# Kernel optimization log

Measured on AMD Instinct MI355X. Metric: run time of the kernel, lower is better.

Reference implementation:

```python
import jax, jax.numpy as jnp
import numpy as np

THRESH = 0.7  # similarity_threshold from __init__
EPS = 1e-8    # torch cosine_similarity eps


def setup_inputs() -> dict:
    key = jax.random.key(0)
    ks = jax.random.split(key, 7)
    B, D, F, H, M, NMEM = 65536, 512, 10, 512, 256, 1024
    return {
        "query_features": jax.random.normal(ks[0], (B, D), jnp.float32),
        "B_mat": jax.random.normal(ks[1], (D, F), jnp.float32),
        "W1": jax.random.normal(ks[2], (2 * F, H), jnp.float32) * 0.05,
        "b1": jax.random.normal(ks[3], (H,), jnp.float32) * 0.01,
        "W2": jax.random.normal(ks[4], (H, M), jnp.float32) * 0.05,
        "b2": jax.random.normal(ks[5], (M,), jnp.float32) * 0.01,
        "memory_bank": jax.random.normal(ks[6], (NMEM, M), jnp.float32),
    }


def reference(query_features, B_mat, W1, b1, W2, b2, memory_bank):
    # Fourier features (eq. 8): [B, 2F]
    xp = query_features @ B_mat
    ff = jnp.concatenate([jnp.sin(xp), jnp.cos(xp)], axis=-1)
    # memory_net MLP -> query vectors [B, M]
    h = jax.nn.relu(ff @ W1 + b1)
    q = h @ W2 + b2
    # cosine similarity q vs memory bank (torch semantics: dot / max(|a||b|, eps))
    qn = jnp.linalg.norm(q, axis=-1, keepdims=True)          # [B,1]
    mn = jnp.linalg.norm(memory_bank, axis=-1, keepdims=True)  # [N,1]
    sim = (q @ memory_bank.T) / jnp.maximum(qn * mn.T, EPS)   # [B,N]
    max_sim = jnp.max(sim, axis=1)                            # [B]
    max_idx = jnp.argmax(sim, axis=1)                         # [B]
    relevant = memory_bank[max_idx]                           # [B,M] gather
    relevant = jnp.where((max_sim < THRESH)[:, None], 0.0, relevant)
    return relevant
```

## Files before the change

### kernel.cpp

```cpp
#include <hip/hip_runtime.h>
#include <hip/hip_bf16.h>


typedef __attribute__((ext_vector_type(8))) short short8;
typedef __attribute__((ext_vector_type(4))) float f32x4;

#define MFMA(a, b, c) __builtin_amdgcn_mfma_f32_16x16x32_bf16((a), (b), (c), 0, 0, 0)

static __device__ __forceinline__ short bfb(float f) {
  return (short)__builtin_bit_cast(unsigned short, __float2bfloat16(f));
}
static __device__ __forceinline__ unsigned short bf16bits(float f) {
  return __builtin_bit_cast(unsigned short, __float2bfloat16(f));
}
static __device__ __forceinline__ float sel10(const float a[10], int i) {
  float v = a[0];
#pragma unroll
  for (int j = 1; j < 10; ++j) v = (i == j) ? a[j] : v;
  return v;
}

typedef const __attribute__((address_space(1))) unsigned int* gas_p;
typedef __attribute__((address_space(3))) unsigned int* las_p;
static __device__ __forceinline__ void async16(const void* g, void* l) {
  __builtin_amdgcn_global_load_lds((gas_p)g, (las_p)l, 16, 0, 0);
}

__global__ __launch_bounds__(256) void prep_ff_kernel(
    const float* __restrict__ W1, const float* __restrict__ b1,
    const float* __restrict__ W2, const float* __restrict__ mem,
    const float* __restrict__ query, const float* __restrict__ Bmat,
    __hip_bfloat16* __restrict__ W1p, __hip_bfloat16* __restrict__ W2p,
    __hip_bfloat16* __restrict__ Mp, __hip_bfloat16* __restrict__ ff) {
  __shared__ __align__(16) float Bl[10 * 512];
  const int b = blockIdx.x, tid = threadIdx.x;
  if (b < 16) {
    float* invl = Bl;
    const int w = tid >> 6, lane = tid & 63, g = lane >> 4, jj = lane & 15;
    {
      int r = w * 16 + jj;
      const float4* m4 = (const float4*)(mem + (size_t)(b * 64 + r) * 256);
      float ss = 0.f;
      for (int t = 0; t < 16; ++t) {
        float4 v = m4[g * 16 + t];
        ss += v.x * v.x + v.y * v.y + v.z * v.z + v.w * v.w;
      }
      ss += __shfl_xor(ss, 16);
      ss += __shfl_xor(ss, 32);
      if (g == 0) invl[r] = rsqrtf(fmaxf(ss, 1e-30f));
    }
    __syncthreads();
    for (int u = 0; u < 64; ++u) {
      int t = u * 256 + tid;
      int j = t & 7, lane2 = (t >> 3) & 63, kt = (t >> 9) & 7, nl = t >> 12;
      int g2 = lane2 >> 4, jp = lane2 & 15;
      int nloc = nl * 16 + jp;
      int kap = 32 * kt + 16 * (j >> 2) + 4 * g2 + (j & 3);
      float v = mem[(size_t)(b * 64 + nloc) * 256 + kap] * invl[nloc];
      Mp[(size_t)b * 16384 + t] = __float2bfloat16(v);
    }
  } else if (b == 16) {
    for (int idx = tid; idx < 16384; idx += 256) {
      int j = idx & 7, lane2 = (idx >> 3) & 63, ct = idx >> 9;
      int g2 = lane2 >> 4, jp = lane2 & 15;
      int k = 8 * g2 + j;
      float v = 0.f;
      if (k < 20) v = W1[k * 512 + ct * 16 + jp];
      else if (k == 20) v = b1[ct * 16 + jp];
      W1p[idx] = __float2bfloat16(v);
    }
  } else if (b < 33) {
    int bb = b - 17;
    for (int u = 0; u < 32; ++u) {
      int idx = bb * 8192 + u * 256 + tid;
      int j = idx & 7, lane2 = (idx >> 3) & 63, c = (idx >> 9) & 15, kt = idx >> 13;
      int g2 = lane2 >> 4, jp = lane2 & 15;
      int kap = 32 * kt + 16 * (j >> 2) + 4 * g2 + (j & 3);
      W2p[idx] = __float2bfloat16(W2[(size_t)kap * 256 + c * 16 + jp]);
    }
  } else {
    const int bb = b - 33;
    for (int i = tid; i < 5120; i += 256) {
      int d = i / 10, f = i - d * 10;
      Bl[f * 512 + d] = Bmat[i];
    }
    __syncthreads();
    const int wv = tid >> 6, lane = tid & 63;
    const int g = lane >> 4, jj = lane & 15;
    const long r0 = (long)bb * 32 + (wv * 4 + g) * 2;
    const float4* qa = (const float4*)(query + r0 * 512);
    const float4* qb = (const float4*)(query + (r0 + 1) * 512);

    float acc[2][10];
#pragma unroll
    for (int f = 0; f < 10; ++f) { acc[0][f] = 0.f; acc[1][f] = 0.f; }
#pragma unroll
    for (int k = 0; k < 8; ++k) {
      float4 va = qa[jj + 16 * k];
      float4 vb = qb[jj + 16 * k];
#pragma unroll
      for (int f = 0; f < 10; ++f) {
        float4 bv = *(const float4*)(Bl + f * 512 + 4 * (jj + 16 * k));
        acc[0][f] = fmaf(va.x, bv.x, fmaf(va.y, bv.y, fmaf(va.z, bv.z, fmaf(va.w, bv.w, acc[0][f]))));
        acc[1][f] = fmaf(vb.x, bv.x, fmaf(vb.y, bv.y, fmaf(vb.z, bv.z, fmaf(vb.w, bv.w, acc[1][f]))));
      }
    }
#pragma unroll
    for (int r = 0; r < 2; ++r) {
#pragma unroll
      for (int f = 0; f < 10; ++f) {
        float s = acc[r][f];
        s += __shfl_xor(s, 1); s += __shfl_xor(s, 2);
        s += __shfl_xor(s, 4); s += __shfl_xor(s, 8);
        acc[r][f] = s;
      }
      int base = (jj < 5) ? 2 * jj : 2 * jj - 10;
      float a0 = sel10(acc[r], base);
      float a1 = sel10(acc[r], base + 1);
      float v0 = 0.f, v1 = 0.f;
      if (jj < 5) { v0 = sinf(a0); v1 = sinf(a1); }
      else if (jj < 10) { v0 = cosf(a0); v1 = cosf(a1); }
      else if (jj == 10) { v0 = 1.0f; }
      ushort2 pk;
      pk.x = bf16bits(v0);
      pk.y = bf16bits(v1);
      ((ushort2*)ff)[(r0 + r) * 16 + jj] = pk;
    }
  }
}

#define WAITV(N) asm volatile("s_waitcnt vmcnt(" #N ")" ::: "memory")
#define BAR()                        \
  do {                               \
    __builtin_amdgcn_s_barrier();    \
    asm volatile("" ::: "memory");   \
  } while (0)

#define STAGE_SLAB(s, bi)                                                       \
  do {                                                                          \
    const char* sp_ = ((s) < 32) ? (const char*)W2p + (size_t)(s) * 8192        \
                                 : (const char*)Mp + ((size_t)(s) - 32) * 8192; \
    char* dp_ = lds + 33792 + (bi) * 8192;                                      \
    async16(sp_ + tid * 16, dp_ + tid * 16);                                    \
    async16(sp_ + 4096 + tid * 16, dp_ + 4096 + tid * 16);                      \
  } while (0)

#define G3_EVEN(t, bi)                                                          \
  do {                                                                          \
    const char* buf = lds + 33792 + (bi) * 8192;                                \
    short8 a0 = *(const short8*)(lds + (size_t)(t) * 1024 + lane * 16);         \
    short8 a1 = *(const short8*)(lds + (size_t)((t) + 1) * 1024 + lane * 16);   \
    f32x4 d00 = MFMA(a0, ffq0, z4);                                             \
    f32x4 d01 = MFMA(a1, ffq0, z4);                                             \
    f32x4 d10 = MFMA(a0, ffq1, z4);                                             \
    f32x4 d11 = MFMA(a1, ffq1, z4);                                             \
    _Pragma("unroll") for (int i = 0; i < 4; ++i) {                             \
      hf0[i] = bfb(d00[i] > 0.f ? d00[i] : 0.f);                                \
      hf0[4 + i] = bfb(d01[i] > 0.f ? d01[i] : 0.f);                            \
      hf1[i] = bfb(d10[i] > 0.f ? d10[i] : 0.f);                                \
      hf1[4 + i] = bfb(d11[i] > 0.f ? d11[i] : 0.f);                            \
    }                                                                           \
    _Pragma("unroll") for (int c = 0; c < 8; ++c) {                             \
      short8 bfr = *(const short8*)(buf + c * 1024 + lane * 16);                \
      acc3a[c] = MFMA(bfr, hf0, acc3a[c]);                                      \
      acc3b[c] = MFMA(bfr, hf1, acc3b[c]);                                      \
    }                                                                           \
  } while (0)

#define G3_ODD(bi)                                                              \
  do {                                                                          \
    const char* buf = lds + 33792 + (bi) * 8192;                                \
    _Pragma("unroll") for (int c = 0; c < 8; ++c) {                             \
      short8 bfr = *(const short8*)(buf + c * 1024 + lane * 16);                \
      acc3a[8 + c] = MFMA(bfr, hf0, acc3a[8 + c]);                              \
      acc3b[8 + c] = MFMA(bfr, hf1, acc3b[8 + c]);                              \
    }                                                                           \
  } while (0)

#define G4(t, bi)                                                               \
  do {                                                                          \
    const char* buf = lds + 33792 + (bi) * 8192;                                \
    f32x4 a40 = z4, a41 = z4;                                                   \
    _Pragma("unroll") for (int kt = 0; kt < 8; ++kt) {                          \
      short8 bfr = *(const short8*)(buf + kt * 1024 + lane * 16);               \
      a40 = MFMA(qfrag0[kt], bfr, a40);                                         \
      a41 = MFMA(qfrag1[kt], bfr, a41);                                         \
    }                                                                           \
    const int n_ = ((t) - 32) * 16 + jj;                                        \
    _Pragma("unroll") for (int i = 0; i < 4; ++i) {                             \
      if (a40[i] > runmax0[i]) { runmax0[i] = a40[i]; runidx0[i] = n_; }        \
      if (a41[i] > runmax1[i]) { runmax1[i] = a41[i]; runidx1[i] = n_; }        \
    }                                                                           \
  } while (0)

__global__ __launch_bounds__(256, 2) void mega_kernel(
    const __hip_bfloat16* __restrict__ ff, const __hip_bfloat16* __restrict__ W1p,
    const __hip_bfloat16* __restrict__ W2p, const float* __restrict__ b2,
    const __hip_bfloat16* __restrict__ Mp, const float* __restrict__ mem,
    float* __restrict__ out) {
  __shared__ __align__(16) char lds[66560];
  const int tid = threadIdx.x, w = tid >> 6, lane = tid & 63;
  const int g = lane >> 4, jj = lane & 15;
  const int rowBase = blockIdx.x * 128 + w * 32;
  const f32x4 z4 = {0.f, 0.f, 0.f, 0.f};

  short8 ffq0 = *(const short8*)(ff + (size_t)(rowBase + jj) * 32 + g * 8);
  short8 ffq1 = *(const short8*)(ff + (size_t)(rowBase + 16 + jj) * 32 + g * 8);
  {
    float v = b2[tid];
    *(float*)(lds + 32768 + tid * 4) = v;
  }
#pragma unroll
  for (int r = 0; r < 8; ++r)
    async16((const char*)W1p + r * 4096 + tid * 16, lds + r * 4096 + tid * 16);
  STAGE_SLAB(0, 0);
  STAGE_SLAB(1, 1);
  STAGE_SLAB(2, 2);

  f32x4 acc3a[16], acc3b[16];
#pragma unroll
  for (int c = 0; c < 16; ++c) { acc3a[c] = z4; acc3b[c] = z4; }
  short8 hf0, hf1;

  for (int it = 0; it < 8; ++it) {
    const int t0 = it * 4;
    WAITV(4); BAR(); STAGE_SLAB(t0 + 3, 3); G3_EVEN(t0, 0);
    WAITV(4); BAR(); STAGE_SLAB(t0 + 4, 0); G3_ODD(1);
    WAITV(4); BAR(); STAGE_SLAB(t0 + 5, 1); G3_EVEN(t0 + 2, 2);
    WAITV(4); BAR(); STAGE_SLAB(t0 + 6, 2); G3_ODD(3);
  }

  short8 qfrag0[8], qfrag1[8];
  float invqn0, invqn1;
  {
    const float* b2l = (const float*)(lds + 32768);
    float qn0 = 0.f, qn1 = 0.f;
#pragma unroll
    for (int c = 0; c < 16; ++c) {
      f32x4 bb = *(const f32x4*)(b2l + c * 16 + 4 * g);
#pragma unroll
      for (int i = 0; i < 4; ++i) {
        float v0 = acc3a[c][i] + bb[i];
        float v1 = acc3b[c][i] + bb[i];
        qn0 += v0 * v0;
        qn1 += v1 * v1;
        qfrag0[c >> 1][(c & 1) * 4 + i] = bfb(v0);
        qfrag1[c >> 1][(c & 1) * 4 + i] = bfb(v1);
      }
    }
    qn0 += __shfl_xor(qn0, 16); qn0 += __shfl_xor(qn0, 32);
    qn1 += __shfl_xor(qn1, 16); qn1 += __shfl_xor(qn1, 32);
    invqn0 = rsqrtf(fmaxf(qn0, 1e-30f));
    invqn1 = rsqrtf(fmaxf(qn1, 1e-30f));
  }

  float runmax0[4], runmax1[4];
  int runidx0[4], runidx1[4];
#pragma unroll
  for (int i = 0; i < 4; ++i) {
    runmax0[i] = -1e30f; runidx0[i] = 0;
    runmax1[i] = -1e30f; runidx1[i] = 0;
  }

  for (int it = 0; it < 15; ++it) {
    const int t0 = 32 + it * 4;
    WAITV(4); BAR(); STAGE_SLAB(t0 + 3, 3); G4(t0, 0);
    WAITV(4); BAR(); STAGE_SLAB(t0 + 4, 0); G4(t0 + 1, 1);
    WAITV(4); BAR(); STAGE_SLAB(t0 + 5, 1); G4(t0 + 2, 2);
    WAITV(4); BAR(); STAGE_SLAB(t0 + 6, 2); G4(t0 + 3, 3);
  }
  WAITV(4); BAR(); STAGE_SLAB(95, 3); G4(92, 0);
  WAITV(4); BAR(); G4(93, 1);
  WAITV(2); BAR(); G4(94, 2);
  WAITV(0); BAR(); G4(95, 3);

  const float4* mem4 = (const float4*)mem;
  float4* out4 = (float4*)out;
#pragma unroll
  for (int rt = 0; rt < 2; ++rt) {
    float* rmax = rt ? runmax1 : runmax0;
    int* ridx = rt ? runidx1 : runidx0;
    float iqv = rt ? invqn1 : invqn0;
#pragma unroll
    for (int i = 0; i < 4; ++i) {
#pragma unroll
      for (int o = 1; o < 16; o <<= 1) {
        float v2 = __shfl_xor(rmax[i], o);
        int i2 = __shfl_xor(ridx[i], o);
        if (v2 > rmax[i] || (v2 == rmax[i] && i2 < ridx[i])) {
          rmax[i] = v2;
          ridx[i] = i2;
        }
      }
    }
#pragma unroll
    for (int i = 0; i < 4; ++i) {
      float iq = __shfl(iqv, 4 * g + i, 64);
      float ms = rmax[i] * iq;
      int s = (ms < 0.7f) ? -1 : ridx[i];
      size_t row = (size_t)rowBase + rt * 16 + 4 * g + i;
#pragma unroll
      for (int cq = 0; cq < 4; ++cq) {
        int col = cq * 16 + jj;
        float4 v = {0.f, 0.f, 0.f, 0.f};
        if (s >= 0) v = mem4[(size_t)s * 64 + col];
        out4[row * 64 + col] = v;
      }
    }
  }
}

extern "C" void kernel_launch(void* const* d_in, const int* in_sizes, int n_in,
                              void* d_out, int out_size, void* d_ws, size_t ws_size,
                              hipStream_t stream) {
  const float* query = (const float*)d_in[0];
  const float* Bmat = (const float*)d_in[1];
  const float* W1 = (const float*)d_in[2];
  const float* b1 = (const float*)d_in[3];
  const float* W2 = (const float*)d_in[4];
  const float* b2 = (const float*)d_in[5];
  const float* mem = (const float*)d_in[6];
  float* out = (float*)d_out;

  char* ws = (char*)d_ws;
  __hip_bfloat16* ff = (__hip_bfloat16*)ws;
  __hip_bfloat16* Mp = (__hip_bfloat16*)(ws + 4194304);
  __hip_bfloat16* W2p = (__hip_bfloat16*)(ws + 4194304 + 524288);
  __hip_bfloat16* W1p = (__hip_bfloat16*)(ws + 4194304 + 786432);

  prep_ff_kernel<<<dim3(2081), dim3(256), 0, stream>>>(W1, b1, W2, mem, query,
                                                       Bmat, W1p, W2p, Mp, ff);
  mega_kernel<<<dim3(512), dim3(256), 0, stream>>>(ff, W1p, W2p, b2, Mp, mem, out);
}
```

Baseline: 95.75 us.

## Fuse Fourier-feature projection into mega kernel and shrink prep kernel

Moves the query @ B_mat projection and the sin/cos feature computation out of the 2048-block prep kernel and into the start of the main kernel. Each wave now computes features for its own 32 rows and hands them to the MFMA fragments through LDS. The prep kernel only writes a transposed B matrix to global memory and repacks the weights, which removes the ff buffer write and read and most of the prep kernel's work. In exchange, the large query read now happens inside a 512-block kernel during its prologue, so it may overlap less well with the other work. LDS per block grows and a full vmcnt wait is added before the main loop.

Result: slower. 123.2 us (+28.6%).

```diff
diff --git a/kernel.cpp b/kernel.cpp
--- a/kernel.cpp
+++ b/kernel.cpp
@@ -26,16 +26,15 @@
   __builtin_amdgcn_global_load_lds((gas_p)g, (las_p)l, 16, 0, 0);
 }
 
-__global__ __launch_bounds__(256) void prep_ff_kernel(
+__global__ __launch_bounds__(256) void prep_kernel(
     const float* __restrict__ W1, const float* __restrict__ b1,
     const float* __restrict__ W2, const float* __restrict__ mem,
-    const float* __restrict__ query, const float* __restrict__ Bmat,
-    __hip_bfloat16* __restrict__ W1p, __hip_bfloat16* __restrict__ W2p,
-    __hip_bfloat16* __restrict__ Mp, __hip_bfloat16* __restrict__ ff) {
-  __shared__ __align__(16) float Bl[10 * 512];
+    const float* __restrict__ Bmat, __hip_bfloat16* __restrict__ W1p,
+    __hip_bfloat16* __restrict__ W2p, __hip_bfloat16* __restrict__ Mp,
+    float* __restrict__ Bt) {
   const int b = blockIdx.x, tid = threadIdx.x;
   if (b < 16) {
-    float* invl = Bl;
+    __shared__ float invl[64];
     const int w = tid >> 6, lane = tid & 63, g = lane >> 4, jj = lane & 15;
     {
       int r = w * 16 + jj;
@@ -69,7 +68,12 @@
       else if (k == 20) v = b1[ct * 16 + jp];
       W1p[idx] = __float2bfloat16(v);
     }
-  } else if (b < 33) {
+  } else if (b == 33) {
+    for (int idx = tid; idx < 5120; idx += 256) {
+      int f = idx >> 9, d = idx & 511;
+      Bt[idx] = Bmat[d * 10 + f];
+    }
+  } else {
     int bb = b - 17;
     for (int u = 0; u < 32; ++u) {
       int idx = bb * 8192 + u * 256 + tid;
@@ -77,54 +81,6 @@
       int g2 = lane2 >> 4, jp = lane2 & 15;
       int kap = 32 * kt + 16 * (j >> 2) + 4 * g2 + (j & 3);
       W2p[idx] = __float2bfloat16(W2[(size_t)kap * 256 + c * 16 + jp]);
-    }
-  } else {
-    const int bb = b - 33;
-    for (int i = tid; i < 5120; i += 256) {
-      int d = i / 10, f = i - d * 10;
-      Bl[f * 512 + d] = Bmat[i];
-    }
-    __syncthreads();
-    const int wv = tid >> 6, lane = tid & 63;
-    const int g = lane >> 4, jj = lane & 15;
-    const long r0 = (long)bb * 32 + (wv * 4 + g) * 2;
-    const float4* qa = (const float4*)(query + r0 * 512);
-    const float4* qb = (const float4*)(query + (r0 + 1) * 512);
-
-    float acc[2][10];
-#pragma unroll
-    for (int f = 0; f < 10; ++f) { acc[0][f] = 0.f; acc[1][f] = 0.f; }
-#pragma unroll
-    for (int k = 0; k < 8; ++k) {
-      float4 va = qa[jj + 16 * k];
-      float4 vb = qb[jj + 16 * k];
-#pragma unroll
-      for (int f = 0; f < 10; ++f) {
-        float4 bv = *(const float4*)(Bl + f * 512 + 4 * (jj + 16 * k));
-        acc[0][f] = fmaf(va.x, bv.x, fmaf(va.y, bv.y, fmaf(va.z, bv.z, fmaf(va.w, bv.w, acc[0][f]))));
-        acc[1][f] = fmaf(vb.x, bv.x, fmaf(vb.y, bv.y, fmaf(vb.z, bv.z, fmaf(vb.w, bv.w, acc[1][f]))));
-      }
-    }
-#pragma unroll
-    for (int r = 0; r < 2; ++r) {
-#pragma unroll
-      for (int f = 0; f < 10; ++f) {
-        float s = acc[r][f];
-        s += __shfl_xor(s, 1); s += __shfl_xor(s, 2);
-        s += __shfl_xor(s, 4); s += __shfl_xor(s, 8);
-        acc[r][f] = s;
-      }
-      int base = (jj < 5) ? 2 * jj : 2 * jj - 10;
-      float a0 = sel10(acc[r], base);
-      float a1 = sel10(acc[r], base + 1);
-      float v0 = 0.f, v1 = 0.f;
-      if (jj < 5) { v0 = sinf(a0); v1 = sinf(a1); }
-      else if (jj < 10) { v0 = cosf(a0); v1 = cosf(a1); }
-      else if (jj == 10) { v0 = 1.0f; }
-      ushort2 pk;
-      pk.x = bf16bits(v0);
-      pk.y = bf16bits(v1);
-      ((ushort2*)ff)[(r0 + r) * 16 + jj] = pk;
     }
   }
 }
@@ -194,18 +150,16 @@
   } while (0)
 
 __global__ __launch_bounds__(256, 2) void mega_kernel(
-    const __hip_bfloat16* __restrict__ ff, const __hip_bfloat16* __restrict__ W1p,
-    const __hip_bfloat16* __restrict__ W2p, const float* __restrict__ b2,
-    const __hip_bfloat16* __restrict__ Mp, const float* __restrict__ mem,
-    float* __restrict__ out) {
-  __shared__ __align__(16) char lds[66560];
+    const float* __restrict__ query, const float* __restrict__ Bt,
+    const __hip_bfloat16* __restrict__ W1p, const __hip_bfloat16* __restrict__ W2p,
+    const float* __restrict__ b2, const __hip_bfloat16* __restrict__ Mp,
+    const float* __restrict__ mem, float* __restrict__ out) {
+  __shared__ __align__(16) char lds[76800];
   const int tid = threadIdx.x, w = tid >> 6, lane = tid & 63;
   const int g = lane >> 4, jj = lane & 15;
   const int rowBase = blockIdx.x * 128 + w * 32;
   const f32x4 z4 = {0.f, 0.f, 0.f, 0.f};
 
-  short8 ffq0 = *(const short8*)(ff + (size_t)(rowBase + jj) * 32 + g * 8);
-  short8 ffq1 = *(const short8*)(ff + (size_t)(rowBase + 16 + jj) * 32 + g * 8);
   {
     float v = b2[tid];
     *(float*)(lds + 32768 + tid * 4) = v;
@@ -216,6 +170,60 @@
   STAGE_SLAB(0, 0);
   STAGE_SLAB(1, 1);
   STAGE_SLAB(2, 2);
+
+  char* ffT = lds + 66560 + w * 2560;
+  {
+    float acc[8][10];
+#pragma unroll
+    for (int rr = 0; rr < 8; ++rr)
+#pragma unroll
+      for (int f = 0; f < 10; ++f) acc[rr][f] = 0.f;
+
+    const float4* q4 = (const float4*)query + (size_t)(rowBase + g * 8) * 128;
+    const float4* bt4 = (const float4*)Bt;
+#pragma unroll 2
+    for (int kk = 0; kk < 8; ++kk) {
+      float4 qv[8];
+#pragma unroll
+      for (int rr = 0; rr < 8; ++rr) qv[rr] = q4[(size_t)rr * 128 + jj + 16 * kk];
+#pragma unroll
+      for (int f = 0; f < 10; ++f) {
+        float4 bv = bt4[f * 128 + jj + 16 * kk];
+#pragma unroll
+        for (int rr = 0; rr < 8; ++rr)
+          acc[rr][f] = fmaf(qv[rr].x, bv.x,
+                       fmaf(qv[rr].y, bv.y,
+                       fmaf(qv[rr].z, bv.z, fmaf(qv[rr].w, bv.w, acc[rr][f]))));
+      }
+    }
+#pragma unroll
+    for (int rr = 0; rr < 8; ++rr) {
+#pragma unroll
+      for (int f = 0; f < 10; ++f) {
+        float s = acc[rr][f];
+        s += __shfl_xor(s, 1); s += __shfl_xor(s, 2);
+        s += __shfl_xor(s, 4); s += __shfl_xor(s, 8);
+        acc[rr][f] = s;
+      }
+      int base = (jj < 5) ? 2 * jj : 2 * jj - 10;
+      float a0 = sel10(acc[rr], base);
+      float a1 = sel10(acc[rr], base + 1);
+      float v0 = 0.f, v1 = 0.f;
+      if (jj < 5) { v0 = sinf(a0); v1 = sinf(a1); }
+      else if (jj < 10) { v0 = cosf(a0); v1 = cosf(a1); }
+      else if (jj == 10) { v0 = 1.0f; }
+      ushort2 pk;
+      pk.x = bf16bits(v0);
+      pk.y = bf16bits(v1);
+      *(ushort2*)(ffT + (g * 8 + rr) * 80 + jj * 4) = pk;
+    }
+  }
+  asm volatile("s_waitcnt lgkmcnt(0)" ::: "memory");
+  __builtin_amdgcn_sched_barrier(0);
+  short8 ffq0 = *(const short8*)(ffT + jj * 80 + g * 16);
+  short8 ffq1 = *(const short8*)(ffT + (16 + jj) * 80 + g * 16);
+
+  asm volatile("s_waitcnt vmcnt(0)" ::: "memory");
 
   f32x4 acc3a[16], acc3b[16];
 #pragma unroll
@@ -323,12 +331,13 @@
   float* out = (float*)d_out;
 
   char* ws = (char*)d_ws;
-  __hip_bfloat16* ff = (__hip_bfloat16*)ws;
-  __hip_bfloat16* Mp = (__hip_bfloat16*)(ws + 4194304);
-  __hip_bfloat16* W2p = (__hip_bfloat16*)(ws + 4194304 + 524288);
-  __hip_bfloat16* W1p = (__hip_bfloat16*)(ws + 4194304 + 786432);
-
-  prep_ff_kernel<<<dim3(2081), dim3(256), 0, stream>>>(W1, b1, W2, mem, query,
-                                                       Bmat, W1p, W2p, Mp, ff);
-  mega_kernel<<<dim3(512), dim3(256), 0, stream>>>(ff, W1p, W2p, b2, Mp, mem, out);
-}
+  __hip_bfloat16* Mp = (__hip_bfloat16*)ws;
+  __hip_bfloat16* W2p = (__hip_bfloat16*)(ws + 524288);
+  __hip_bfloat16* W1p = (__hip_bfloat16*)(ws + 786432);
+  float* Bt = (float*)(ws + 819200);
+
+  prep_kernel<<<dim3(34), dim3(256), 0, stream>>>(W1, b1, W2, mem, Bmat,
+                                                  W1p, W2p, Mp, Bt);
+  mega_kernel<<<dim3(512), dim3(256), 0, stream>>>(query, Bt, W1p, W2p, b2, Mp,
+                                                   mem, out);
+}
```

## Switch second MLP layer and similarity GEMM from bf16 to fp8 MFMA

Applied to the files above, without the earlier changes.

Quantizes W2, the normalized memory bank, the hidden activations and the query vectors to FP8 (e4m3-style, software conversion) and runs the second MLP layer and the cosine-similarity GEMM with fp8 MFMA. This halves the staged slab count and LDS traffic, and each fp8 MFMA covers the same K per instruction. The operand layouts are repacked so each 16-byte LDS read feeds two MFMAs. The cost is a hand-written float-to-fp8 conversion on the activations and a large precision loss, which can flip argmax and threshold decisions against the fp32 reference.

Result: slower. 105.9 us (+10.6%).

```diff
diff --git a/kernel.cpp b/kernel.cpp
--- a/kernel.cpp
+++ b/kernel.cpp
@@ -4,14 +4,28 @@
 
 typedef __attribute__((ext_vector_type(8))) short short8;
 typedef __attribute__((ext_vector_type(4))) float f32x4;
+typedef __attribute__((ext_vector_type(2))) long i64x2;
 
 #define MFMA(a, b, c) __builtin_amdgcn_mfma_f32_16x16x32_bf16((a), (b), (c), 0, 0, 0)
+#define MFMA8(a, b, c) __builtin_amdgcn_mfma_f32_16x16x32_fp8_fp8((long)(a), (long)(b), (c), 0, 0, 0)
 
 static __device__ __forceinline__ short bfb(float f) {
   return (short)__builtin_bit_cast(unsigned short, __float2bfloat16(f));
 }
 static __device__ __forceinline__ unsigned short bf16bits(float f) {
   return __builtin_bit_cast(unsigned short, __float2bfloat16(f));
+}
+static __device__ __forceinline__ unsigned f8(float x) {
+  unsigned u = __builtin_bit_cast(unsigned, x);
+  unsigned s = (u >> 24) & 0x80;
+  int e = (int)((u >> 23) & 0xff) - 127;
+  if (e < -6) {
+    float ax = __builtin_fabsf(x);
+    int mm = (int)(ax * 512.f + 0.5f);
+    return s | (unsigned)mm;
+  }
+  if (e > 8) return s | 0x7e;
+  return s | ((unsigned)(e + 7) << 3) | ((u >> 20) & 7);
 }
 static __device__ __forceinline__ float sel10(const float a[10], int i) {
   float v = a[0];
@@ -30,8 +44,8 @@
     const float* __restrict__ W1, const float* __restrict__ b1,
     const float* __restrict__ W2, const float* __restrict__ mem,
     const float* __restrict__ query, const float* __restrict__ Bmat,
-    __hip_bfloat16* __restrict__ W1p, __hip_bfloat16* __restrict__ W2p,
-    __hip_bfloat16* __restrict__ Mp, __hip_bfloat16* __restrict__ ff) {
+    __hip_bfloat16* __restrict__ W1p, unsigned char* __restrict__ W2p8,
+    unsigned char* __restrict__ Mp8, __hip_bfloat16* __restrict__ ff) {
   __shared__ __align__(16) float Bl[10 * 512];
   const int b = blockIdx.x, tid = threadIdx.x;
   if (b < 16) {
@@ -52,12 +66,14 @@
     __syncthreads();
     for (int u = 0; u < 64; ++u) {
       int t = u * 256 + tid;
-      int j = t & 7, lane2 = (t >> 3) & 63, kt = (t >> 9) & 7, nl = t >> 12;
+      int j = t & 7, kk = (t >> 3) & 1, lane2 = (t >> 4) & 63;
+      int ktp = (t >> 10) & 3, ngl = t >> 12;
       int g2 = lane2 >> 4, jp = lane2 & 15;
-      int nloc = nl * 16 + jp;
-      int kap = 32 * kt + 16 * (j >> 2) + 4 * g2 + (j & 3);
-      float v = mem[(size_t)(b * 64 + nloc) * 256 + kap] * invl[nloc];
-      Mp[(size_t)b * 16384 + t] = __float2bfloat16(v);
+      int kt = ktp * 2 + kk;
+      int k = 32 * kt + 16 * (j >> 2) + 4 * g2 + (j & 3);
+      int nloc = ngl * 16 + jp;
+      float v = mem[(size_t)(b * 64 + nloc) * 256 + k] * invl[nloc];
+      Mp8[(size_t)b * 16384 + t] = (unsigned char)f8(v);
     }
   } else if (b == 16) {
     for (int idx = tid; idx < 16384; idx += 256) {
@@ -70,13 +86,14 @@
       W1p[idx] = __float2bfloat16(v);
     }
   } else if (b < 33) {
-    int bb = b - 17;
+    int kt = b - 17;
     for (int u = 0; u < 32; ++u) {
-      int idx = bb * 8192 + u * 256 + tid;
-      int j = idx & 7, lane2 = (idx >> 3) & 63, c = (idx >> 9) & 15, kt = idx >> 13;
+      int t = u * 256 + tid;
+      int j = t & 7, cc = (t >> 3) & 1, lane2 = (t >> 4) & 63, cpair = t >> 10;
       int g2 = lane2 >> 4, jp = lane2 & 15;
-      int kap = 32 * kt + 16 * (j >> 2) + 4 * g2 + (j & 3);
-      W2p[idx] = __float2bfloat16(W2[(size_t)kap * 256 + c * 16 + jp]);
+      int k = 32 * kt + 16 * (j >> 2) + 4 * g2 + (j & 3);
+      int col = (cpair * 2 + cc) * 16 + jp;
+      W2p8[(size_t)kt * 8192 + t] = (unsigned char)f8(W2[(size_t)k * 256 + col]);
     }
   } else {
     const int bb = b - 33;
@@ -136,67 +153,66 @@
     asm volatile("" ::: "memory");   \
   } while (0)
 
-#define STAGE_SLAB(s, bi)                                                       \
-  do {                                                                          \
-    const char* sp_ = ((s) < 32) ? (const char*)W2p + (size_t)(s) * 8192        \
-                                 : (const char*)Mp + ((size_t)(s) - 32) * 8192; \
-    char* dp_ = lds + 33792 + (bi) * 8192;                                      \
-    async16(sp_ + tid * 16, dp_ + tid * 16);                                    \
-    async16(sp_ + 4096 + tid * 16, dp_ + 4096 + tid * 16);                      \
+#define STAGE_SLAB(s, bi)                                                        \
+  do {                                                                           \
+    const char* sp_ = ((s) < 16) ? (const char*)W2p8 + (size_t)(s) * 8192        \
+                                 : (const char*)Mp8 + ((size_t)(s) - 16) * 8192; \
+    char* dp_ = lds + 33792 + (bi) * 8192;                                       \
+    async16(sp_ + tid * 16, dp_ + tid * 16);                                     \
+    async16(sp_ + 4096 + tid * 16, dp_ + 4096 + tid * 16);                       \
   } while (0)
 
-#define G3_EVEN(t, bi)                                                          \
-  do {                                                                          \
-    const char* buf = lds + 33792 + (bi) * 8192;                                \
-    short8 a0 = *(const short8*)(lds + (size_t)(t) * 1024 + lane * 16);         \
-    short8 a1 = *(const short8*)(lds + (size_t)((t) + 1) * 1024 + lane * 16);   \
-    f32x4 d00 = MFMA(a0, ffq0, z4);                                             \
-    f32x4 d01 = MFMA(a1, ffq0, z4);                                             \
-    f32x4 d10 = MFMA(a0, ffq1, z4);                                             \
-    f32x4 d11 = MFMA(a1, ffq1, z4);                                             \
-    _Pragma("unroll") for (int i = 0; i < 4; ++i) {                             \
-      hf0[i] = bfb(d00[i] > 0.f ? d00[i] : 0.f);                                \
-      hf0[4 + i] = bfb(d01[i] > 0.f ? d01[i] : 0.f);                            \
-      hf1[i] = bfb(d10[i] > 0.f ? d10[i] : 0.f);                                \
-      hf1[4 + i] = bfb(d11[i] > 0.f ? d11[i] : 0.f);                            \
-    }                                                                           \
-    _Pragma("unroll") for (int c = 0; c < 8; ++c) {                             \
-      short8 bfr = *(const short8*)(buf + c * 1024 + lane * 16);                \
-      acc3a[c] = MFMA(bfr, hf0, acc3a[c]);                                      \
-      acc3b[c] = MFMA(bfr, hf1, acc3b[c]);                                      \
-    }                                                                           \
+#define G3(t, bi)                                                             \
+  do {                                                                        \
+    const char* buf = lds + 33792 + (bi) * 8192;                              \
+    short8 a0 = *(const short8*)(lds + (size_t)(2 * (t)) * 1024 + lane * 16); \
+    short8 a1 = *(const short8*)(lds + (size_t)(2 * (t) + 1) * 1024 + lane * 16); \
+    f32x4 d00 = MFMA(a0, ffq0, z4);                                           \
+    f32x4 d01 = MFMA(a1, ffq0, z4);                                           \
+    f32x4 d10 = MFMA(a0, ffq1, z4);                                           \
+    f32x4 d11 = MFMA(a1, ffq1, z4);                                           \
+    unsigned lo0 = 0, hi0 = 0, lo1 = 0, hi1 = 0;                              \
+    _Pragma("unroll") for (int i = 0; i < 4; ++i) {                           \
+      lo0 |= f8(fmaxf(d00[i], 0.f)) << (8 * i);                               \
+      hi0 |= f8(fmaxf(d01[i], 0.f)) << (8 * i);                               \
+      lo1 |= f8(fmaxf(d10[i], 0.f)) << (8 * i);                               \
+      hi1 |= f8(fmaxf(d11[i], 0.f)) << (8 * i);                               \
+    }                                                                         \
+    long hf0 = (long)(((unsigned long)hi0 << 32) | lo0);                      \
+    long hf1 = (long)(((unsigned long)hi1 << 32) | lo1);                      \
+    _Pragma("unroll") for (int cp = 0; cp < 8; ++cp) {                        \
+      i64x2 wfr = *(const i64x2*)(buf + cp * 1024 + lane * 16);               \
+      acc3a[2 * cp] = MFMA8(wfr[0], hf0, acc3a[2 * cp]);                      \
+      acc3b[2 * cp] = MFMA8(wfr[0], hf1, acc3b[2 * cp]);                      \
+      acc3a[2 * cp + 1] = MFMA8(wfr[1], hf0, acc3a[2 * cp + 1]);              \
+      acc3b[2 * cp + 1] = MFMA8(wfr[1], hf1, acc3b[2 * cp + 1]);              \
+    }                                                                         \
   } while (0)
 
-#define G3_ODD(bi)                                                              \
-  do {                                                                          \
-    const char* buf = lds + 33792 + (bi) * 8192;                                \
-    _Pragma("unroll") for (int c = 0; c < 8; ++c) {                             \
-      short8 bfr = *(const short8*)(buf + c * 1024 + lane * 16);                \
-      acc3a[8 + c] = MFMA(bfr, hf0, acc3a[8 + c]);                              \
-      acc3b[8 + c] = MFMA(bfr, hf1, acc3b[8 + c]);                              \
-    }                                                                           \
-  } while (0)
-
-#define G4(t, bi)                                                               \
-  do {                                                                          \
-    const char* buf = lds + 33792 + (bi) * 8192;                                \
-    f32x4 a40 = z4, a41 = z4;                                                   \
-    _Pragma("unroll") for (int kt = 0; kt < 8; ++kt) {                          \
-      short8 bfr = *(const short8*)(buf + kt * 1024 + lane * 16);               \
-      a40 = MFMA(qfrag0[kt], bfr, a40);                                         \
-      a41 = MFMA(qfrag1[kt], bfr, a41);                                         \
-    }                                                                           \
-    const int n_ = ((t) - 32) * 16 + jj;                                        \
-    _Pragma("unroll") for (int i = 0; i < 4; ++i) {                             \
-      if (a40[i] > runmax0[i]) { runmax0[i] = a40[i]; runidx0[i] = n_; }        \
-      if (a41[i] > runmax1[i]) { runmax1[i] = a41[i]; runidx1[i] = n_; }        \
-    }                                                                           \
+#define G4PAIR(t, bi)                                                         \
+  do {                                                                        \
+    const char* buf = lds + 33792 + (bi) * 8192;                              \
+    _Pragma("unroll") for (int ngl = 0; ngl < 2; ++ngl) {                     \
+      f32x4 a40 = z4, a41 = z4;                                               \
+      _Pragma("unroll") for (int ktp = 0; ktp < 4; ++ktp) {                   \
+        i64x2 mfr = *(const i64x2*)(buf + ngl * 4096 + ktp * 1024 + lane * 16); \
+        a40 = MFMA8(q0[2 * ktp], mfr[0], a40);                                \
+        a41 = MFMA8(q1[2 * ktp], mfr[0], a41);                                \
+        a40 = MFMA8(q0[2 * ktp + 1], mfr[1], a40);                            \
+        a41 = MFMA8(q1[2 * ktp + 1], mfr[1], a41);                            \
+      }                                                                       \
+      const int n_ = (((t) - 16) * 2 + ngl) * 16 + jj;                        \
+      _Pragma("unroll") for (int i = 0; i < 4; ++i) {                         \
+        if (a40[i] > runmax0[i]) { runmax0[i] = a40[i]; runidx0[i] = n_; }    \
+        if (a41[i] > runmax1[i]) { runmax1[i] = a41[i]; runidx1[i] = n_; }    \
+      }                                                                       \
+    }                                                                         \
   } while (0)
 
 __global__ __launch_bounds__(256, 2) void mega_kernel(
     const __hip_bfloat16* __restrict__ ff, const __hip_bfloat16* __restrict__ W1p,
-    const __hip_bfloat16* __restrict__ W2p, const float* __restrict__ b2,
-    const __hip_bfloat16* __restrict__ Mp, const float* __restrict__ mem,
+    const unsigned char* __restrict__ W2p8, const float* __restrict__ b2,
+    const unsigned char* __restrict__ Mp8, const float* __restrict__ mem,
     float* __restrict__ out) {
   __shared__ __align__(16) char lds[66560];
   const int tid = threadIdx.x, w = tid >> 6, lane = tid & 63;
@@ -220,33 +236,44 @@
   f32x4 acc3a[16], acc3b[16];
 #pragma unroll
   for (int c = 0; c < 16; ++c) { acc3a[c] = z4; acc3b[c] = z4; }
-  short8 hf0, hf1;
-
-  for (int it = 0; it < 8; ++it) {
+
+  for (int it = 0; it < 4; ++it) {
     const int t0 = it * 4;
-    WAITV(4); BAR(); STAGE_SLAB(t0 + 3, 3); G3_EVEN(t0, 0);
-    WAITV(4); BAR(); STAGE_SLAB(t0 + 4, 0); G3_ODD(1);
-    WAITV(4); BAR(); STAGE_SLAB(t0 + 5, 1); G3_EVEN(t0 + 2, 2);
-    WAITV(4); BAR(); STAGE_SLAB(t0 + 6, 2); G3_ODD(3);
-  }
-
-  short8 qfrag0[8], qfrag1[8];
+    WAITV(4); BAR(); STAGE_SLAB(t0 + 3, 3); G3(t0, 0);
+    WAITV(4); BAR(); STAGE_SLAB(t0 + 4, 0); G3(t0 + 1, 1);
+    WAITV(4); BAR(); STAGE_SLAB(t0 + 5, 1); G3(t0 + 2, 2);
+    WAITV(4); BAR(); STAGE_SLAB(t0 + 6, 2); G3(t0 + 3, 3);
+  }
+
+  long q0[8], q1[8];
   float invqn0, invqn1;
   {
     const float* b2l = (const float*)(lds + 32768);
     float qn0 = 0.f, qn1 = 0.f;
 #pragma unroll
-    for (int c = 0; c < 16; ++c) {
-      f32x4 bb = *(const f32x4*)(b2l + c * 16 + 4 * g);
-#pragma unroll
-      for (int i = 0; i < 4; ++i) {
-        float v0 = acc3a[c][i] + bb[i];
-        float v1 = acc3b[c][i] + bb[i];
-        qn0 += v0 * v0;
-        qn1 += v1 * v1;
-        qfrag0[c >> 1][(c & 1) * 4 + i] = bfb(v0);
-        qfrag1[c >> 1][(c & 1) * 4 + i] = bfb(v1);
-      }
+    for (int kt = 0; kt < 8; ++kt) {
+      unsigned w0 = 0, w1 = 0, w2 = 0, w3 = 0;
+#pragma unroll
+      for (int half = 0; half < 2; ++half) {
+        const int c = 2 * kt + half;
+        f32x4 bb = *(const f32x4*)(b2l + c * 16 + 4 * g);
+#pragma unroll
+        for (int i = 0; i < 4; ++i) {
+          float v0 = acc3a[c][i] + bb[i];
+          float v1 = acc3b[c][i] + bb[i];
+          qn0 += v0 * v0;
+          qn1 += v1 * v1;
+          if (half == 0) {
+            w0 |= f8(v0) << (8 * i);
+            w2 |= f8(v1) << (8 * i);
+          } else {
+            w1 |= f8(v0) << (8 * i);
+            w3 |= f8(v1) << (8 * i);
+          }
+        }
+      }
+      q0[kt] = (long)(((unsigned long)w1 << 32) | w0);
+      q1[kt] = (long)(((unsigned long)w3 << 32) | w2);
     }
     qn0 += __shfl_xor(qn0, 16); qn0 += __shfl_xor(qn0, 32);
     qn1 += __shfl_xor(qn1, 16); qn1 += __shfl_xor(qn1, 32);
@@ -262,17 +289,17 @@
     runmax1[i] = -1e30f; runidx1[i] = 0;
   }
 
-  for (int it = 0; it < 15; ++it) {
-    const int t0 = 32 + it * 4;
-    WAITV(4); BAR(); STAGE_SLAB(t0 + 3, 3); G4(t0, 0);
-    WAITV(4); BAR(); STAGE_SLAB(t0 + 4, 0); G4(t0 + 1, 1);
-    WAITV(4); BAR(); STAGE_SLAB(t0 + 5, 1); G4(t0 + 2, 2);
-    WAITV(4); BAR(); STAGE_SLAB(t0 + 6, 2); G4(t0 + 3, 3);
-  }
-  WAITV(4); BAR(); STAGE_SLAB(95, 3); G4(92, 0);
-  WAITV(4); BAR(); G4(93, 1);
-  WAITV(2); BAR(); G4(94, 2);
-  WAITV(0); BAR(); G4(95, 3);
+  for (int it = 0; it < 7; ++it) {
+    const int t0 = 16 + it * 4;
+    WAITV(4); BAR(); STAGE_SLAB(t0 + 3, 3); G4PAIR(t0, 0);
+    WAITV(4); BAR(); STAGE_SLAB(t0 + 4, 0); G4PAIR(t0 + 1, 1);
+    WAITV(4); BAR(); STAGE_SLAB(t0 + 5, 1); G4PAIR(t0 + 2, 2);
+    WAITV(4); BAR(); STAGE_SLAB(t0 + 6, 2); G4PAIR(t0 + 3, 3);
+  }
+  WAITV(4); BAR(); STAGE_SLAB(47, 3); G4PAIR(44, 0);
+  WAITV(4); BAR(); G4PAIR(45, 1);
+  WAITV(2); BAR(); G4PAIR(46, 2);
+  WAITV(0); BAR(); G4PAIR(47, 3);
 
   const float4* mem4 = (const float4*)mem;
   float4* out4 = (float4*)out;
@@ -324,11 +351,11 @@
 
   char* ws = (char*)d_ws;
   __hip_bfloat16* ff = (__hip_bfloat16*)ws;
-  __hip_bfloat16* Mp = (__hip_bfloat16*)(ws + 4194304);
-  __hip_bfloat16* W2p = (__hip_bfloat16*)(ws + 4194304 + 524288);
-  __hip_bfloat16* W1p = (__hip_bfloat16*)(ws + 4194304 + 786432);
+  unsigned char* Mp8 = (unsigned char*)(ws + 4194304);
+  unsigned char* W2p8 = (unsigned char*)(ws + 4194304 + 262144);
+  __hip_bfloat16* W1p = (__hip_bfloat16*)(ws + 4194304 + 393216);
 
   prep_ff_kernel<<<dim3(2081), dim3(256), 0, stream>>>(W1, b1, W2, mem, query,
-                                                       Bmat, W1p, W2p, Mp, ff);
-  mega_kernel<<<dim3(512), dim3(256), 0, stream>>>(ff, W1p, W2p, b2, Mp, mem, out);
-}
+                                                       Bmat, W1p, W2p8, Mp8, ff);
+  mega_kernel<<<dim3(512), dim3(256), 0, stream>>>(ff, W1p, W2p8, b2, Mp8, mem, out);
+}
```

## Double block to 512 threads with 16 rows per wave

Applied to the files above, without the earlier changes.

Each block now runs 8 waves instead of 4, and each wave handles 16 query rows instead of 32. This halves the per-wave accumulators and MFMA work. Each shared W2 and memory-bank slab is staged with one async copy per thread instead of two. The aim is to cut register pressure and raise occupancy and latency hiding. In exchange, each LDS fragment read now feeds half as many MFMAs, so LDS traffic per FLOP roughly doubles. Barriers also now span more waves.

New measurement: 100.4 us. +4.9%, slower.

```diff
diff --git a/kernel.cpp b/kernel.cpp
--- a/kernel.cpp
+++ b/kernel.cpp
@@ -140,9 +140,7 @@
   do {                                                                          \
     const char* sp_ = ((s) < 32) ? (const char*)W2p + (size_t)(s) * 8192        \
                                  : (const char*)Mp + ((size_t)(s) - 32) * 8192; \
-    char* dp_ = lds + 33792 + (bi) * 8192;                                      \
-    async16(sp_ + tid * 16, dp_ + tid * 16);                                    \
-    async16(sp_ + 4096 + tid * 16, dp_ + 4096 + tid * 16);                      \
+    async16(sp_ + tid * 16, lds + 33792 + (bi) * 8192 + tid * 16);              \
   } while (0)
 
 #define G3_EVEN(t, bi)                                                          \
@@ -152,18 +150,13 @@
     short8 a1 = *(const short8*)(lds + (size_t)((t) + 1) * 1024 + lane * 16);   \
     f32x4 d00 = MFMA(a0, ffq0, z4);                                             \
     f32x4 d01 = MFMA(a1, ffq0, z4);                                             \
-    f32x4 d10 = MFMA(a0, ffq1, z4);                                             \
-    f32x4 d11 = MFMA(a1, ffq1, z4);                                             \
     _Pragma("unroll") for (int i = 0; i < 4; ++i) {                             \
       hf0[i] = bfb(d00[i] > 0.f ? d00[i] : 0.f);                                \
       hf0[4 + i] = bfb(d01[i] > 0.f ? d01[i] : 0.f);                            \
-      hf1[i] = bfb(d10[i] > 0.f ? d10[i] : 0.f);                                \
-      hf1[4 + i] = bfb(d11[i] > 0.f ? d11[i] : 0.f);                            \
     }                                                                           \
     _Pragma("unroll") for (int c = 0; c < 8; ++c) {                             \
       short8 bfr = *(const short8*)(buf + c * 1024 + lane * 16);                \
       acc3a[c] = MFMA(bfr, hf0, acc3a[c]);                                      \
-      acc3b[c] = MFMA(bfr, hf1, acc3b[c]);                                      \
     }                                                                           \
   } while (0)
 
@@ -173,27 +166,24 @@
     _Pragma("unroll") for (int c = 0; c < 8; ++c) {                             \
       short8 bfr = *(const short8*)(buf + c * 1024 + lane * 16);                \
       acc3a[8 + c] = MFMA(bfr, hf0, acc3a[8 + c]);                              \
-      acc3b[8 + c] = MFMA(bfr, hf1, acc3b[8 + c]);                              \
     }                                                                           \
   } while (0)
 
 #define G4(t, bi)                                                               \
   do {                                                                          \
     const char* buf = lds + 33792 + (bi) * 8192;                                \
-    f32x4 a40 = z4, a41 = z4;                                                   \
+    f32x4 a40 = z4;                                                             \
     _Pragma("unroll") for (int kt = 0; kt < 8; ++kt) {                          \
       short8 bfr = *(const short8*)(buf + kt * 1024 + lane * 16);               \
       a40 = MFMA(qfrag0[kt], bfr, a40);                                         \
-      a41 = MFMA(qfrag1[kt], bfr, a41);                                         \
     }                                                                           \
     const int n_ = ((t) - 32) * 16 + jj;                                        \
     _Pragma("unroll") for (int i = 0; i < 4; ++i) {                             \
       if (a40[i] > runmax0[i]) { runmax0[i] = a40[i]; runidx0[i] = n_; }        \
-      if (a41[i] > runmax1[i]) { runmax1[i] = a41[i]; runidx1[i] = n_; }        \
-    }                                                                           \
-  } while (0)
-
-__global__ __launch_bounds__(256, 2) void mega_kernel(
+    }                                                                           \
+  } while (0)
+
+__global__ __launch_bounds__(512, 2) void mega_kernel(
     const __hip_bfloat16* __restrict__ ff, const __hip_bfloat16* __restrict__ W1p,
     const __hip_bfloat16* __restrict__ W2p, const float* __restrict__ b2,
     const __hip_bfloat16* __restrict__ Mp, const float* __restrict__ mem,
@@ -201,111 +191,97 @@
   __shared__ __align__(16) char lds[66560];
   const int tid = threadIdx.x, w = tid >> 6, lane = tid & 63;
   const int g = lane >> 4, jj = lane & 15;
-  const int rowBase = blockIdx.x * 128 + w * 32;
+  const int rowBase = blockIdx.x * 128 + w * 16;
   const f32x4 z4 = {0.f, 0.f, 0.f, 0.f};
 
   short8 ffq0 = *(const short8*)(ff + (size_t)(rowBase + jj) * 32 + g * 8);
-  short8 ffq1 = *(const short8*)(ff + (size_t)(rowBase + 16 + jj) * 32 + g * 8);
-  {
+  if (tid < 256) {
     float v = b2[tid];
     *(float*)(lds + 32768 + tid * 4) = v;
   }
 #pragma unroll
-  for (int r = 0; r < 8; ++r)
-    async16((const char*)W1p + r * 4096 + tid * 16, lds + r * 4096 + tid * 16);
+  for (int r = 0; r < 4; ++r)
+    async16((const char*)W1p + r * 8192 + tid * 16, lds + r * 8192 + tid * 16);
   STAGE_SLAB(0, 0);
   STAGE_SLAB(1, 1);
   STAGE_SLAB(2, 2);
 
-  f32x4 acc3a[16], acc3b[16];
-#pragma unroll
-  for (int c = 0; c < 16; ++c) { acc3a[c] = z4; acc3b[c] = z4; }
-  short8 hf0, hf1;
+  f32x4 acc3a[16];
+#pragma unroll
+  for (int c = 0; c < 16; ++c) acc3a[c] = z4;
+  short8 hf0;
 
   for (int it = 0; it < 8; ++it) {
     const int t0 = it * 4;
-    WAITV(4); BAR(); STAGE_SLAB(t0 + 3, 3); G3_EVEN(t0, 0);
-    WAITV(4); BAR(); STAGE_SLAB(t0 + 4, 0); G3_ODD(1);
-    WAITV(4); BAR(); STAGE_SLAB(t0 + 5, 1); G3_EVEN(t0 + 2, 2);
-    WAITV(4); BAR(); STAGE_SLAB(t0 + 6, 2); G3_ODD(3);
-  }
-
-  short8 qfrag0[8], qfrag1[8];
-  float invqn0, invqn1;
+    WAITV(2); BAR(); STAGE_SLAB(t0 + 3, 3); G3_EVEN(t0, 0);
+    WAITV(2); BAR(); STAGE_SLAB(t0 + 4, 0); G3_ODD(1);
+    WAITV(2); BAR(); STAGE_SLAB(t0 + 5, 1); G3_EVEN(t0 + 2, 2);
+    WAITV(2); BAR(); STAGE_SLAB(t0 + 6, 2); G3_ODD(3);
+  }
+
+  short8 qfrag0[8];
+  float invqn0;
   {
     const float* b2l = (const float*)(lds + 32768);
-    float qn0 = 0.f, qn1 = 0.f;
+    float qn0 = 0.f;
 #pragma unroll
     for (int c = 0; c < 16; ++c) {
       f32x4 bb = *(const f32x4*)(b2l + c * 16 + 4 * g);
 #pragma unroll
       for (int i = 0; i < 4; ++i) {
         float v0 = acc3a[c][i] + bb[i];
-        float v1 = acc3b[c][i] + bb[i];
         qn0 += v0 * v0;
-        qn1 += v1 * v1;
         qfrag0[c >> 1][(c & 1) * 4 + i] = bfb(v0);
-        qfrag1[c >> 1][(c & 1) * 4 + i] = bfb(v1);
-      }
-    }
-    qn0 += __shfl_xor(qn0, 16); qn0 += __shfl_xor(qn0, 32);
-    qn1 += __shfl_xor(qn1, 16); qn1 += __shfl_xor(qn1, 32);
+      }
+    }
+    qn0 += __shfl_xor(qn0, 16);
+    qn0 += __shfl_xor(qn0, 32);
     invqn0 = rsqrtf(fmaxf(qn0, 1e-30f));
-    invqn1 = rsqrtf(fmaxf(qn1, 1e-30f));
-  }
-
-  float runmax0[4], runmax1[4];
-  int runidx0[4], runidx1[4];
-#pragma unroll
-  for (int i = 0; i < 4; ++i) {
-    runmax0[i] = -1e30f; runidx0[i] = 0;
-    runmax1[i] = -1e30f; runidx1[i] = 0;
-  }
+  }
+
+  float runmax0[4];
+  int runidx0[4];
+#pragma unroll
+  for (int i = 0; i < 4; ++i) { runmax0[i] = -1e30f; runidx0[i] = 0; }
 
   for (int it = 0; it < 15; ++it) {
     const int t0 = 32 + it * 4;
-    WAITV(4); BAR(); STAGE_SLAB(t0 + 3, 3); G4(t0, 0);
-    WAITV(4); BAR(); STAGE_SLAB(t0 + 4, 0); G4(t0 + 1, 1);
-    WAITV(4); BAR(); STAGE_SLAB(t0 + 5, 1); G4(t0 + 2, 2);
-    WAITV(4); BAR(); STAGE_SLAB(t0 + 6, 2); G4(t0 + 3, 3);
-  }
-  WAITV(4); BAR(); STAGE_SLAB(95, 3); G4(92, 0);
-  WAITV(4); BAR(); G4(93, 1);
-  WAITV(2); BAR(); G4(94, 2);
+    WAITV(2); BAR(); STAGE_SLAB(t0 + 3, 3); G4(t0, 0);
+    WAITV(2); BAR(); STAGE_SLAB(t0 + 4, 0); G4(t0 + 1, 1);
+    WAITV(2); BAR(); STAGE_SLAB(t0 + 5, 1); G4(t0 + 2, 2);
+    WAITV(2); BAR(); STAGE_SLAB(t0 + 6, 2); G4(t0 + 3, 3);
+  }
+  WAITV(2); BAR(); STAGE_SLAB(95, 3); G4(92, 0);
+  WAITV(2); BAR(); G4(93, 1);
+  WAITV(1); BAR(); G4(94, 2);
   WAITV(0); BAR(); G4(95, 3);
 
   const float4* mem4 = (const float4*)mem;
   float4* out4 = (float4*)out;
 #pragma unroll
-  for (int rt = 0; rt < 2; ++rt) {
-    float* rmax = rt ? runmax1 : runmax0;
-    int* ridx = rt ? runidx1 : runidx0;
-    float iqv = rt ? invqn1 : invqn0;
-#pragma unroll
-    for (int i = 0; i < 4; ++i) {
-#pragma unroll
-      for (int o = 1; o < 16; o <<= 1) {
-        float v2 = __shfl_xor(rmax[i], o);
-        int i2 = __shfl_xor(ridx[i], o);
-        if (v2 > rmax[i] || (v2 == rmax[i] && i2 < ridx[i])) {
-          rmax[i] = v2;
-          ridx[i] = i2;
-        }
-      }
-    }
-#pragma unroll
-    for (int i = 0; i < 4; ++i) {
-      float iq = __shfl(iqv, 4 * g + i, 64);
-      float ms = rmax[i] * iq;
-      int s = (ms < 0.7f) ? -1 : ridx[i];
-      size_t row = (size_t)rowBase + rt * 16 + 4 * g + i;
-#pragma unroll
-      for (int cq = 0; cq < 4; ++cq) {
-        int col = cq * 16 + jj;
-        float4 v = {0.f, 0.f, 0.f, 0.f};
-        if (s >= 0) v = mem4[(size_t)s * 64 + col];
-        out4[row * 64 + col] = v;
-      }
+  for (int i = 0; i < 4; ++i) {
+#pragma unroll
+    for (int o = 1; o < 16; o <<= 1) {
+      float v2 = __shfl_xor(runmax0[i], o);
+      int i2 = __shfl_xor(runidx0[i], o);
+      if (v2 > runmax0[i] || (v2 == runmax0[i] && i2 < runidx0[i])) {
+        runmax0[i] = v2;
+        runidx0[i] = i2;
+      }
+    }
+  }
+#pragma unroll
+  for (int i = 0; i < 4; ++i) {
+    float iq = __shfl(invqn0, 4 * g + i, 64);
+    float ms = runmax0[i] * iq;
+    int s = (ms < 0.7f) ? -1 : runidx0[i];
+    size_t row = (size_t)rowBase + 4 * g + i;
+#pragma unroll
+    for (int cq = 0; cq < 4; ++cq) {
+      int col = cq * 16 + jj;
+      float4 v = {0.f, 0.f, 0.f, 0.f};
+      if (s >= 0) v = mem4[(size_t)s * 64 + col];
+      out4[row * 64 + col] = v;
     }
   }
 }
@@ -330,5 +306,5 @@
 
   prep_ff_kernel<<<dim3(2081), dim3(256), 0, stream>>>(W1, b1, W2, mem, query,
                                                        Bmat, W1p, W2p, Mp, ff);
-  mega_kernel<<<dim3(512), dim3(256), 0, stream>>>(ff, W1p, W2p, b2, Mp, mem, out);
-}
+  mega_kernel<<<dim3(512), dim3(512), 0, stream>>>(ff, W1p, W2p, b2, Mp, mem, out);
+}
```
